# Kernel tuning notes

Measured on AMD Instinct MI355X. Metric: run time of the kernel, lower is better.

Reference implementation:

```python
import jax, jax.numpy as jnp
import numpy as np

TOPK = 10
NUM_CLASSES = 80
ALPHA = 0.5
BETA = 6.0
EPS = 1e-16


def _iou_xyxy(b1, b2):
    # b1, b2 broadcastable [..., 4] in xyxy; matches bbox_iou(xywh=False, CIoU=False)
    b1_x1, b1_y1, b1_x2, b1_y2 = b1[..., 0], b1[..., 1], b1[..., 2], b1[..., 3]
    b2_x1, b2_y1, b2_x2, b2_y2 = b2[..., 0], b2[..., 1], b2[..., 2], b2[..., 3]
    inter = jnp.clip(jnp.minimum(b1_x2, b2_x2) - jnp.maximum(b1_x1, b2_x1), 0) * \
            jnp.clip(jnp.minimum(b1_y2, b2_y2) - jnp.maximum(b1_y1, b2_y1), 0)
    w1, h1 = b1_x2 - b1_x1, b1_y2 - b1_y1 + EPS
    w2, h2 = b2_x2 - b2_x1, b2_y2 - b2_y1 + EPS
    union = w1 * h1 + w2 * h2 - inter + EPS
    return inter / union


def _assign_one(pd_s, pd_b, gt_l, gt_b, m, anc):
    # pd_s [A,C], pd_b [A,4], gt_l [N,1], gt_b [N,4], m [N,1] bool, anc [A,2]
    A = pd_s.shape[0]
    N = gt_l.shape[0]
    valid = m[:, 0]                                  # [N] padded-gt mask
    labels = gt_l[:, 0]                              # [N]
    scores = pd_s[:, labels]                         # [A,N] gather per-gt class score
    ious = _iou_xyxy(gt_b[None, :, :], pd_b[:, None, :])   # [A,N]
    align = scores ** ALPHA * ious ** BETA           # [A,N]
    # anchor-center-inside-gt test
    lt = anc[:, None, :] - gt_b[None, :, :2]         # [A,N,2]
    rb = gt_b[None, :, 2:] - anc[:, None, :]         # [A,N,2]
    in_gts = jnp.concatenate([lt, rb], axis=-1).min(axis=-1) > 0  # [A,N]
    amf = align * in_gts                             # align_metric_filter
    amf = jnp.where(valid[None, :], amf, 0.0)        # padded gts contribute nothing
    # top-k anchors per gt (over anchor dim)
    topk_idx = jax.lax.top_k(amf.T, TOPK)[1]         # [N,TOPK]
    mask_topk = jnp.zeros((N, A), dtype=bool).at[jnp.arange(N)[:, None], topk_idx].set(True).T  # [A,N]
    mask_pos = mask_topk & in_gts & valid[None, :]   # [A,N]
    fg = mask_pos.any(axis=1)                        # [A]
    # argmax over valid gts (padded columns pushed below any valid amf >= 0)
    amf_arg = jnp.where(valid[None, :], amf, -1.0)
    gt_idx = jnp.argmax(amf_arg, axis=1)             # [A]
    t_labels = jnp.where(fg, labels[gt_idx], NUM_CLASSES).astype(jnp.int32)
    t_bboxes = jnp.where(fg[:, None], gt_b[gt_idx], 0.0)
    am_max = jnp.clip(jnp.max(amf_arg, axis=1), 0.0)  # [A]
    BIG = jnp.float32(1e30)
    mn = jnp.min(jnp.where(fg, am_max, BIG))
    mx = jnp.max(jnp.where(fg, am_max, -BIG))
    norm = (am_max - mn) / (mx - mn + 1e-9)
    onehot = jax.nn.one_hot(t_labels, NUM_CLASSES, dtype=pd_s.dtype)  # label==C -> all-zero row
    t_scores = jnp.where(fg[:, None], onehot * norm[:, None], 0.0)
    return t_labels, t_bboxes, t_scores, fg


def setup_inputs() -> dict:
    key = jax.random.key(0)
    B, A, N, C = 32, 8400, 64, NUM_CLASSES
    ks = jax.random.split(key, 8)
    pd_scores = jax.random.uniform(ks[0], (B, A, C), dtype=jnp.float32)
    xy1 = jax.random.uniform(ks[1], (B, A, 2), dtype=jnp.float32) * 600.0
    wh = jax.random.uniform(ks[2], (B, A, 2), dtype=jnp.float32) * 60.0 + 4.0
    pd_bboxes = jnp.concatenate([xy1, xy1 + wh], axis=-1)
    anc_points = jax.random.uniform(ks[3], (A, 2), dtype=jnp.float32) * 640.0
    gxy1 = jax.random.uniform(ks[4], (B, N, 2), dtype=jnp.float32) * 500.0
    gwh = jax.random.uniform(ks[5], (B, N, 2), dtype=jnp.float32) * 140.0 + 20.0
    gt_bboxes = jnp.concatenate([gxy1, gxy1 + gwh], axis=-1)
    gt_labels = jax.random.randint(ks[6], (B, N, 1), 0, C, dtype=jnp.int32)
    counts = jax.random.randint(ks[7], (B,), 1, N + 1)
    mask_gt = (jnp.arange(N)[None, :] < counts[:, None])[..., None]  # [B,N,1] bool
    return {"pd_scores": pd_scores, "pd_bboxes": pd_bboxes, "anc_points": anc_points,
            "gt_labels": gt_labels, "gt_bboxes": gt_bboxes, "mask_gt": mask_gt}


def reference(pd_scores, pd_bboxes, anc_points, gt_labels, gt_bboxes, mask_gt):
    return jax.vmap(_assign_one, in_axes=(0, 0, 0, 0, 0, None))(
        pd_scores, pd_bboxes, gt_labels, gt_bboxes, mask_gt, anc_points)
```

## Files before the change

kernel.cpp:

```cpp
#include <hip/hip_runtime.h>

#define A_N 8400
#define B_N 32
#define NGT 64
#define NC  80
#define BA  (B_N * A_N)
#define NCOL (B_N * NGT)

typedef float f4 __attribute__((ext_vector_type(4)));

__global__ __launch_bounds__(256) void k_init(int* __restrict__ cnts,
                                              unsigned* __restrict__ mn_g,
                                              unsigned* __restrict__ mx_g) {
  int tid = threadIdx.x;
  for (int i = tid; i < NCOL; i += 256) cnts[i] = 0;
  if (tid < B_N) {
    mn_g[tid] = __float_as_uint(1e30f);
    mx_g[tid] = 0u;
  }
}

__global__ __launch_bounds__(256) void k_pairs(
    const float* __restrict__ pd_s, const float* __restrict__ pd_b,
    const float* __restrict__ anc, const int* __restrict__ gt_l,
    const float* __restrict__ gt_b, const int* __restrict__ mgt,
    unsigned long long* __restrict__ lists, int* __restrict__ cnts, int cap,
    unsigned long long* __restrict__ recs) {
#pragma clang fp contract(off)
  int b = blockIdx.y, tid = threadIdx.x;
  int a0 = blockIdx.x * 256, a = a0 + tid;
  bool av = a < A_N;

  __shared__ float4 gb_s[NGT];
  __shared__ int lab_s[NGT];
  __shared__ float4 pb_s[256];
  __shared__ unsigned long long key_s[256];
  __shared__ unsigned short wl[256 * 64];
  __shared__ int wl_cnt;
  __shared__ int cnt_sh;

  if (tid < NGT) {
    gb_s[tid] = ((const float4*)gt_b)[b * NGT + tid];
    lab_s[tid] = gt_l[b * NGT + tid];
    unsigned long long m = __ballot(mgt[b * NGT + tid] != 0);
    if (tid == 0) cnt_sh = __popcll(m);
  }
  float4 pb = av ? ((const float4*)pd_b)[(size_t)b * A_N + a]
                 : make_float4(0.f, 0.f, 0.f, 0.f);
  float2 ap = av ? ((const float2*)anc)[a] : make_float2(-1e30f, -1e30f);
  pb_s[tid] = pb;
  key_s[tid] = (unsigned long long)(63 << 1);
  if (tid == 0) wl_cnt = 0;
  __syncthreads();
  int cnt = cnt_sh;

  if (av) {
    for (int n = 0; n < cnt; n++) {
      float4 gb = gb_s[n];
      float mn = fminf(fminf(ap.x - gb.x, ap.y - gb.y),
                       fminf(gb.z - ap.x, gb.w - ap.y));
      float iwr = fminf(gb.z, pb.z) - fmaxf(gb.x, pb.x);
      float ihr = fminf(gb.w, pb.w) - fmaxf(gb.y, pb.y);
      if (mn > 0.0f && iwr > 0.0f && ihr > 0.0f) {
        int p = atomicAdd(&wl_cnt, 1);
        wl[p] = (unsigned short)((tid << 6) | n);
      }
    }
  }
  __syncthreads();
  int m = wl_cnt;

  for (int i = tid; i < m; i += 256) {
    int e = wl[i];
    int al = e >> 6, n = e & 63;
    int ag = a0 + al;
    float4 gb = gb_s[n];
    float4 pbl = pb_s[al];
    float iw = fmaxf(fminf(gb.z, pbl.z) - fmaxf(gb.x, pbl.x), 0.0f);
    float ih = fmaxf(fminf(gb.w, pbl.w) - fmaxf(gb.y, pbl.y), 0.0f);
    float inter = iw * ih;
    float w1 = gb.z - gb.x, h1 = (gb.w - gb.y) + 1e-16f;
    float w2 = pbl.z - pbl.x, h2 = (pbl.w - pbl.y) + 1e-16f;
    float uni = ((w1 * h1 + w2 * h2) - inter) + 1e-16f;
    float iou = inter / uni;
    float sc = pd_s[((size_t)b * A_N + ag) * NC + (size_t)lab_s[n]];
    float v = sqrtf(sc) * powf(iou, 6.0f);
    if (v > 0.0f) {
      unsigned vb = __float_as_uint(v);
      int col = b * NGT + n;
      int pos = atomicAdd(&cnts[col], 1);
      if (pos < cap) {
        lists[(size_t)col * cap + pos] =
            ((unsigned long long)vb << 32) |
            (unsigned long long)(0xFFFFFFFFu - (unsigned)ag);
      }
      atomicMax(&key_s[al], ((unsigned long long)vb << 32) |
                                (unsigned long long)((63 - n) << 1));
    }
  }
  __syncthreads();

  if (av) recs[(size_t)b * A_N + a] = key_s[tid];
}

__global__ __launch_bounds__(64) void k_topk(
    const unsigned long long* __restrict__ lists, const int* __restrict__ cnts,
    int cap, const int* __restrict__ mgt, const float* __restrict__ anc,
    const float* __restrict__ gt_b, unsigned long long* __restrict__ recs,
    unsigned* __restrict__ mn_g, unsigned* __restrict__ mx_g) {
  int b = blockIdx.x, n = blockIdx.y, tid = threadIdx.x;
  if (mgt[b * NGT + n] == 0) return;
  int col = b * NGT + n;
  int P = cnts[col];
  if (P > cap) P = cap;
  const unsigned long long* list = lists + (size_t)col * cap;
  unsigned* recw = (unsigned*)recs;

  const unsigned MN_ID = __float_as_uint(1e30f);
  unsigned loc_mn = MN_ID, loc_mx = 0u;

  if (P >= 10) {
    unsigned long long top[10];
#pragma unroll
    for (int j = 0; j < 10; j++) top[j] = 0ull;
    for (int i = tid; i < P; i += 64) {
      unsigned long long key = list[i];
#pragma unroll
      for (int j = 0; j < 10; j++) {
        if (key > top[j]) { unsigned long long t = top[j]; top[j] = key; key = t; }
      }
    }
    for (int r = 0; r < 10; r++) {
      unsigned long long g = top[0];
#pragma unroll
      for (int off = 32; off >= 1; off >>= 1) {
        unsigned long long o = __shfl_xor(g, off, 64);
        g = (o > g) ? o : g;
      }
      if (top[0] == g) {
#pragma unroll
        for (int j = 0; j < 9; j++) top[j] = top[j + 1];
        top[9] = 0ull;
      }
      if (tid == r) {
        size_t idx = (size_t)b * A_N +
                     (size_t)(0xFFFFFFFFu - (unsigned)(g & 0xFFFFFFFFull));
        atomicOr(&recw[2 * idx], 1u);
        unsigned u = recw[2 * idx + 1];
        loc_mn = (u < loc_mn) ? u : loc_mn;
        loc_mx = (u > loc_mx) ? u : loc_mx;
      }
    }
  } else {
    int my_a = -1;
    if (tid < P)
      my_a = (int)(0xFFFFFFFFu - (unsigned)(list[tid] & 0xFFFFFFFFull));
    if (tid < P) {
      size_t idx = (size_t)b * A_N + my_a;
      atomicOr(&recw[2 * idx], 1u);
      unsigned u = recw[2 * idx + 1];
      loc_mn = (u < loc_mn) ? u : loc_mn;
      loc_mx = (u > loc_mx) ? u : loc_mx;
    }
    bool is_pos = false;
    for (int i = 0; i < P; i++) {
      int ai = __shfl(my_a, i, 64);
      is_pos |= (ai == tid);
    }
    bool cand = (tid < 19) && !is_pos;
    unsigned long long fm = __ballot(cand);
    int rank = __popcll(fm & ((1ull << tid) - 1ull));
    if (cand && rank < 10 - P) {
      float4 gb = ((const float4*)gt_b)[b * NGT + n];
      float2 ap = ((const float2*)anc)[tid];
      float mn = fminf(fminf(ap.x - gb.x, ap.y - gb.y),
                       fminf(gb.z - ap.x, gb.w - ap.y));
      if (mn > 0.0f) {
        size_t idx = (size_t)b * A_N + tid;
        atomicOr(&recw[2 * idx], 1u);
        unsigned u = recw[2 * idx + 1];
        loc_mn = (u < loc_mn) ? u : loc_mn;
        loc_mx = (u > loc_mx) ? u : loc_mx;
      }
    }
  }

#pragma unroll
  for (int off = 32; off >= 1; off >>= 1) {
    unsigned o1 = __shfl_xor(loc_mn, off, 64);
    loc_mn = (o1 < loc_mn) ? o1 : loc_mn;
    unsigned o2 = __shfl_xor(loc_mx, off, 64);
    loc_mx = (o2 > loc_mx) ? o2 : loc_mx;
  }
  if (tid == 0 && loc_mn != MN_ID) {
    atomicMin(&mn_g[b], loc_mn);
    atomicMax(&mx_g[b], loc_mx);
  }
}

__global__ __launch_bounds__(256) void k_fin(
    const int* __restrict__ gt_l, const float* __restrict__ gt_b,
    const unsigned long long* __restrict__ recs,
    const unsigned* __restrict__ mn_g, const unsigned* __restrict__ mx_g,
    float* __restrict__ out) {
  int b = blockIdx.y;
  int a = blockIdx.x * 256 + threadIdx.x;
  if (a >= A_N) return;
  size_t i = (size_t)b * A_N + a;
  unsigned long long rec = recs[i];
  bool fg = (rec & 1ull) != 0;
  int bi = 63 - (int)((rec >> 1) & 63ull);
  int lab = gt_l[b * NGT + bi];

  out[i] = fg ? (float)lab : (float)NC;
  if (fg) {
    float amx = __uint_as_float((unsigned)(rec >> 32));
    float mn = __uint_as_float(mn_g[b]);
    float mx = __uint_as_float(mx_g[b]);
    float norm = (amx - mn) / ((mx - mn) + 1e-9f);
    float4 t = ((const float4*)gt_b)[b * NGT + bi];
    f4 bb = {t.x, t.y, t.z, t.w};
    ((f4*)(out + BA))[i] = bb;
    out[(size_t)85 * BA + i] = 1.0f;
    out[(size_t)5 * BA + i * NC + (size_t)lab] = norm;
  }
}

extern "C" void kernel_launch(void* const* d_in, const int* in_sizes, int n_in,
                              void* d_out, int out_size, void* d_ws,
                              size_t ws_size, hipStream_t stream) {
  const float* pd_s = (const float*)d_in[0];
  const float* pd_b = (const float*)d_in[1];
  const float* anc  = (const float*)d_in[2];
  const int*   gt_l = (const int*)d_in[3];
  const float* gt_b = (const float*)d_in[4];
  const int*   mgt  = (const int*)d_in[5];

  float* out = (float*)d_out;
  char* ws = (char*)d_ws;

  const size_t REC_BYTES = (size_t)BA * 8;
  size_t small_bytes = REC_BYTES + (size_t)NCOL * 4 + 256;
  size_t avail = (ws_size > small_bytes) ? (ws_size - small_bytes) : 0;
  int cap = (int)(avail / ((size_t)NCOL * 8));
  if (cap > 4096) cap = 4096;
  if (cap < 1) cap = 1;

  unsigned long long* lists = (unsigned long long*)ws;
  char* sb = ws + (size_t)NCOL * 8 * cap;
  unsigned long long* recs = (unsigned long long*)sb;
  int*      cnts = (int*)(sb + REC_BYTES);
  unsigned* mn_g = (unsigned*)(sb + REC_BYTES + (size_t)NCOL * 4);
  unsigned* mx_g = mn_g + B_N;

  hipMemsetAsync(out + BA, 0, (size_t)85 * BA * 4, stream);

  dim3 g2((A_N + 255) / 256, B_N);
  k_init<<<1, 256, 0, stream>>>(cnts, mn_g, mx_g);
  k_pairs<<<g2, 256, 0, stream>>>(pd_s, pd_b, anc, gt_l, gt_b, mgt, lists,
                                  cnts, cap, recs);
  k_topk<<<dim3(B_N, NGT), 64, 0, stream>>>(lists, cnts, cap, mgt, anc, gt_b,
                                            recs, mn_g, mx_g);
  k_fin<<<g2, 256, 0, stream>>>(gt_l, gt_b, recs, mn_g, mx_g, out);
}
```

Baseline: 182.9 us.

## Fuse pair, top-k and finalize stages into one cooperative kernel with grid syncs

Replaces the init, pairs, top-k and finalize kernels, plus the large output memset, with a single cooperative kernel of 512 blocks. 192 blocks zero the output with nontemporal stores while the other blocks run the pair tiles, so the zeroing overlaps the pair work. Grid-wide syncs then separate the top-k stage, where each block handles 4 columns with one wavefront each, from the finalize stage. This removes launch gaps and the separate memset pass. In exchange, it relies on all 512 blocks being co-resident and pays for two grid barriers; the min initialiser also changes from 1e30 bits to 0xFFFFFFFF.

```diff
diff --git a/kernel.cpp b/kernel.cpp
--- a/kernel.cpp
+++ b/kernel.cpp
@@ -1,4 +1,7 @@
 #include <hip/hip_runtime.h>
+#include <hip/hip_cooperative_groups.h>
+
+namespace cg = cooperative_groups;
 
 #define A_N 8400
 #define B_N 32
@@ -6,30 +9,25 @@
 #define NC  80
 #define BA  (B_N * A_N)
 #define NCOL (B_N * NGT)
+#define NBLK 512
+#define ZB   192
+#define PB   (NBLK - ZB)
+#define NTILE (33 * B_N)
+#define ZVEC ((size_t)85 * BA / 4)
 
 typedef float f4 __attribute__((ext_vector_type(4)));
 
-__global__ __launch_bounds__(256) void k_init(int* __restrict__ cnts,
-                                              unsigned* __restrict__ mn_g,
-                                              unsigned* __restrict__ mx_g) {
-  int tid = threadIdx.x;
-  for (int i = tid; i < NCOL; i += 256) cnts[i] = 0;
-  if (tid < B_N) {
-    mn_g[tid] = __float_as_uint(1e30f);
-    mx_g[tid] = 0u;
-  }
-}
-
-__global__ __launch_bounds__(256) void k_pairs(
+__global__ __launch_bounds__(256) void k_fused(
     const float* __restrict__ pd_s, const float* __restrict__ pd_b,
     const float* __restrict__ anc, const int* __restrict__ gt_l,
     const float* __restrict__ gt_b, const int* __restrict__ mgt,
     unsigned long long* __restrict__ lists, int* __restrict__ cnts, int cap,
-    unsigned long long* __restrict__ recs) {
+    unsigned long long* __restrict__ recs, unsigned* __restrict__ mn_g,
+    unsigned* __restrict__ mx_g, float* __restrict__ out) {
 #pragma clang fp contract(off)
-  int b = blockIdx.y, tid = threadIdx.x;
-  int a0 = blockIdx.x * 256, a = a0 + tid;
-  bool av = a < A_N;
+  cg::grid_group grid = cg::this_grid();
+  int tid = threadIdx.x;
+  int bk = blockIdx.x;
 
   __shared__ float4 gb_s[NGT];
   __shared__ int lab_s[NGT];
@@ -39,190 +37,201 @@
   __shared__ int wl_cnt;
   __shared__ int cnt_sh;
 
-  if (tid < NGT) {
-    gb_s[tid] = ((const float4*)gt_b)[b * NGT + tid];
-    lab_s[tid] = gt_l[b * NGT + tid];
-    unsigned long long m = __ballot(mgt[b * NGT + tid] != 0);
-    if (tid == 0) cnt_sh = __popcll(m);
-  }
-  float4 pb = av ? ((const float4*)pd_b)[(size_t)b * A_N + a]
-                 : make_float4(0.f, 0.f, 0.f, 0.f);
-  float2 ap = av ? ((const float2*)anc)[a] : make_float2(-1e30f, -1e30f);
-  pb_s[tid] = pb;
-  key_s[tid] = (unsigned long long)(63 << 1);
-  if (tid == 0) wl_cnt = 0;
-  __syncthreads();
-  int cnt = cnt_sh;
-
-  if (av) {
-    for (int n = 0; n < cnt; n++) {
-      float4 gb = gb_s[n];
-      float mn = fminf(fminf(ap.x - gb.x, ap.y - gb.y),
-                       fminf(gb.z - ap.x, gb.w - ap.y));
-      float iwr = fminf(gb.z, pb.z) - fmaxf(gb.x, pb.x);
-      float ihr = fminf(gb.w, pb.w) - fmaxf(gb.y, pb.y);
-      if (mn > 0.0f && iwr > 0.0f && ihr > 0.0f) {
-        int p = atomicAdd(&wl_cnt, 1);
-        wl[p] = (unsigned short)((tid << 6) | n);
-      }
+  if (bk < ZB) {
+    f4 z = {0.f, 0.f, 0.f, 0.f};
+    f4* dst = (f4*)(out + BA);
+    for (size_t v = (size_t)bk * 256 + tid; v < ZVEC; v += (size_t)ZB * 256)
+      __builtin_nontemporal_store(z, &dst[v]);
+  } else {
+    int pr = bk - ZB;
+    for (int t = pr; t < NTILE; t += PB) {
+      int b = t / 33, bx = t - b * 33;
+      int a0 = bx * 256, a = a0 + tid;
+      bool av = a < A_N;
+
+      if (tid < NGT) {
+        gb_s[tid] = ((const float4*)gt_b)[b * NGT + tid];
+        lab_s[tid] = gt_l[b * NGT + tid];
+        unsigned long long mm = __ballot(mgt[b * NGT + tid] != 0);
+        if (tid == 0) cnt_sh = __popcll(mm);
+      }
+      float4 pb = av ? ((const float4*)pd_b)[(size_t)b * A_N + a]
+                     : make_float4(0.f, 0.f, 0.f, 0.f);
+      float2 ap = av ? ((const float2*)anc)[a] : make_float2(-1e30f, -1e30f);
+      pb_s[tid] = pb;
+      key_s[tid] = (unsigned long long)(63 << 1);
+      if (tid == 0) wl_cnt = 0;
+      __syncthreads();
+      int cnt = cnt_sh;
+
+      if (av) {
+        for (int n = 0; n < cnt; n++) {
+          float4 gb = gb_s[n];
+          float mn = fminf(fminf(ap.x - gb.x, ap.y - gb.y),
+                           fminf(gb.z - ap.x, gb.w - ap.y));
+          float iwr = fminf(gb.z, pb.z) - fmaxf(gb.x, pb.x);
+          float ihr = fminf(gb.w, pb.w) - fmaxf(gb.y, pb.y);
+          if (mn > 0.0f && iwr > 0.0f && ihr > 0.0f) {
+            int p = atomicAdd(&wl_cnt, 1);
+            wl[p] = (unsigned short)((tid << 6) | n);
+          }
+        }
+      }
+      __syncthreads();
+      int m = wl_cnt;
+
+      for (int i = tid; i < m; i += 256) {
+        int e = wl[i];
+        int al = e >> 6, n = e & 63;
+        int ag = a0 + al;
+        float4 gb = gb_s[n];
+        float4 pbl = pb_s[al];
+        float iw = fmaxf(fminf(gb.z, pbl.z) - fmaxf(gb.x, pbl.x), 0.0f);
+        float ih = fmaxf(fminf(gb.w, pbl.w) - fmaxf(gb.y, pbl.y), 0.0f);
+        float inter = iw * ih;
+        float w1 = gb.z - gb.x, h1 = (gb.w - gb.y) + 1e-16f;
+        float w2 = pbl.z - pbl.x, h2 = (pbl.w - pbl.y) + 1e-16f;
+        float uni = ((w1 * h1 + w2 * h2) - inter) + 1e-16f;
+        float iou = inter / uni;
+        float sc = pd_s[((size_t)b * A_N + ag) * NC + (size_t)lab_s[n]];
+        float v = sqrtf(sc) * powf(iou, 6.0f);
+        if (v > 0.0f) {
+          unsigned vb = __float_as_uint(v);
+          int col = b * NGT + n;
+          int pos = atomicAdd(&cnts[col], 1);
+          if (pos < cap) {
+            lists[(size_t)col * cap + pos] =
+                ((unsigned long long)vb << 32) |
+                (unsigned long long)(0xFFFFFFFFu - (unsigned)ag);
+          }
+          atomicMax(&key_s[al], ((unsigned long long)vb << 32) |
+                                    (unsigned long long)((63 - n) << 1));
+        }
+      }
+      __syncthreads();
+      if (av) recs[(size_t)b * A_N + a] = key_s[tid];
     }
   }
-  __syncthreads();
-  int m = wl_cnt;
-
-  for (int i = tid; i < m; i += 256) {
-    int e = wl[i];
-    int al = e >> 6, n = e & 63;
-    int ag = a0 + al;
-    float4 gb = gb_s[n];
-    float4 pbl = pb_s[al];
-    float iw = fmaxf(fminf(gb.z, pbl.z) - fmaxf(gb.x, pbl.x), 0.0f);
-    float ih = fmaxf(fminf(gb.w, pbl.w) - fmaxf(gb.y, pbl.y), 0.0f);
-    float inter = iw * ih;
-    float w1 = gb.z - gb.x, h1 = (gb.w - gb.y) + 1e-16f;
-    float w2 = pbl.z - pbl.x, h2 = (pbl.w - pbl.y) + 1e-16f;
-    float uni = ((w1 * h1 + w2 * h2) - inter) + 1e-16f;
-    float iou = inter / uni;
-    float sc = pd_s[((size_t)b * A_N + ag) * NC + (size_t)lab_s[n]];
-    float v = sqrtf(sc) * powf(iou, 6.0f);
-    if (v > 0.0f) {
-      unsigned vb = __float_as_uint(v);
-      int col = b * NGT + n;
-      int pos = atomicAdd(&cnts[col], 1);
-      if (pos < cap) {
-        lists[(size_t)col * cap + pos] =
-            ((unsigned long long)vb << 32) |
-            (unsigned long long)(0xFFFFFFFFu - (unsigned)ag);
-      }
-      atomicMax(&key_s[al], ((unsigned long long)vb << 32) |
-                                (unsigned long long)((63 - n) << 1));
+
+  __threadfence();
+  grid.sync();
+
+  {
+    int lane = tid & 63;
+    int col = bk * 4 + (tid >> 6);
+    unsigned* recw = (unsigned*)recs;
+    unsigned loc_mn = 0xFFFFFFFFu, loc_mx = 0u;
+    if (mgt[col] != 0) {
+      int b = col >> 6;
+      int P = cnts[col];
+      if (P > cap) P = cap;
+      const unsigned long long* list = lists + (size_t)col * cap;
+
+      if (P >= 10) {
+        unsigned long long top[10];
+#pragma unroll
+        for (int j = 0; j < 10; j++) top[j] = 0ull;
+        for (int i = lane; i < P; i += 64) {
+          unsigned long long key = list[i];
+#pragma unroll
+          for (int j = 0; j < 10; j++) {
+            if (key > top[j]) { unsigned long long tt = top[j]; top[j] = key; key = tt; }
+          }
+        }
+        for (int r = 0; r < 10; r++) {
+          unsigned long long g = top[0];
+#pragma unroll
+          for (int off = 32; off >= 1; off >>= 1) {
+            unsigned long long o = __shfl_xor(g, off, 64);
+            g = (o > g) ? o : g;
+          }
+          if (top[0] == g) {
+#pragma unroll
+            for (int j = 0; j < 9; j++) top[j] = top[j + 1];
+            top[9] = 0ull;
+          }
+          if (lane == r) {
+            size_t idx = (size_t)b * A_N +
+                         (size_t)(0xFFFFFFFFu - (unsigned)(g & 0xFFFFFFFFull));
+            atomicOr(&recw[2 * idx], 1u);
+            unsigned u = recw[2 * idx + 1];
+            loc_mn = (u < loc_mn) ? u : loc_mn;
+            loc_mx = (u > loc_mx) ? u : loc_mx;
+          }
+        }
+      } else {
+        int my_a = -1;
+        if (lane < P)
+          my_a = (int)(0xFFFFFFFFu - (unsigned)(list[lane] & 0xFFFFFFFFull));
+        if (lane < P) {
+          size_t idx = (size_t)b * A_N + my_a;
+          atomicOr(&recw[2 * idx], 1u);
+          unsigned u = recw[2 * idx + 1];
+          loc_mn = (u < loc_mn) ? u : loc_mn;
+          loc_mx = (u > loc_mx) ? u : loc_mx;
+        }
+        bool is_pos = false;
+        for (int i = 0; i < P; i++) {
+          int ai = __shfl(my_a, i, 64);
+          is_pos |= (ai == lane);
+        }
+        bool cand = (lane < 19) && !is_pos;
+        unsigned long long fm = __ballot(cand);
+        int rank = __popcll(fm & ((1ull << lane) - 1ull));
+        if (cand && rank < 10 - P) {
+          int n = col & 63;
+          float4 gb = ((const float4*)gt_b)[b * NGT + n];
+          float2 ap = ((const float2*)anc)[lane];
+          float mn = fminf(fminf(ap.x - gb.x, ap.y - gb.y),
+                           fminf(gb.z - ap.x, gb.w - ap.y));
+          if (mn > 0.0f) {
+            size_t idx = (size_t)b * A_N + lane;
+            atomicOr(&recw[2 * idx], 1u);
+            unsigned u = recw[2 * idx + 1];
+            loc_mn = (u < loc_mn) ? u : loc_mn;
+            loc_mx = (u > loc_mx) ? u : loc_mx;
+          }
+        }
+      }
+#pragma unroll
+      for (int off = 32; off >= 1; off >>= 1) {
+        unsigned o1 = __shfl_xor(loc_mn, off, 64);
+        loc_mn = (o1 < loc_mn) ? o1 : loc_mn;
+        unsigned o2 = __shfl_xor(loc_mx, off, 64);
+        loc_mx = (o2 > loc_mx) ? o2 : loc_mx;
+      }
+      if (lane == 0 && loc_mn != 0xFFFFFFFFu) {
+        atomicMin(&mn_g[b], loc_mn);
+        atomicMax(&mx_g[b], loc_mx);
+      }
     }
   }
-  __syncthreads();
-
-  if (av) recs[(size_t)b * A_N + a] = key_s[tid];
-}
-
-__global__ __launch_bounds__(64) void k_topk(
-    const unsigned long long* __restrict__ lists, const int* __restrict__ cnts,
-    int cap, const int* __restrict__ mgt, const float* __restrict__ anc,
-    const float* __restrict__ gt_b, unsigned long long* __restrict__ recs,
-    unsigned* __restrict__ mn_g, unsigned* __restrict__ mx_g) {
-  int b = blockIdx.x, n = blockIdx.y, tid = threadIdx.x;
-  if (mgt[b * NGT + n] == 0) return;
-  int col = b * NGT + n;
-  int P = cnts[col];
-  if (P > cap) P = cap;
-  const unsigned long long* list = lists + (size_t)col * cap;
-  unsigned* recw = (unsigned*)recs;
-
-  const unsigned MN_ID = __float_as_uint(1e30f);
-  unsigned loc_mn = MN_ID, loc_mx = 0u;
-
-  if (P >= 10) {
-    unsigned long long top[10];
-#pragma unroll
-    for (int j = 0; j < 10; j++) top[j] = 0ull;
-    for (int i = tid; i < P; i += 64) {
-      unsigned long long key = list[i];
-#pragma unroll
-      for (int j = 0; j < 10; j++) {
-        if (key > top[j]) { unsigned long long t = top[j]; top[j] = key; key = t; }
+
+  __threadfence();
+  grid.sync();
+
+  for (int t = bk; t < NTILE; t += NBLK) {
+    int b = t / 33, bx = t - b * 33;
+    int a = bx * 256 + tid;
+    if (a < A_N) {
+      size_t i = (size_t)b * A_N + a;
+      unsigned long long rec = recs[i];
+      bool fg = (rec & 1ull) != 0;
+      int bi = 63 - (int)((rec >> 1) & 63ull);
+      int lab = gt_l[b * NGT + bi];
+      out[i] = fg ? (float)lab : (float)NC;
+      if (fg) {
+        float amx = __uint_as_float((unsigned)(rec >> 32));
+        float mn = __uint_as_float(mn_g[b]);
+        float mx = __uint_as_float(mx_g[b]);
+        float norm = (amx - mn) / ((mx - mn) + 1e-9f);
+        float4 tt = ((const float4*)gt_b)[b * NGT + bi];
+        f4 bb = {tt.x, tt.y, tt.z, tt.w};
+        ((f4*)(out + BA))[i] = bb;
+        out[(size_t)85 * BA + i] = 1.0f;
+        out[(size_t)5 * BA + i * NC + (size_t)lab] = norm;
       }
     }
-    for (int r = 0; r < 10; r++) {
-      unsigned long long g = top[0];
-#pragma unroll
-      for (int off = 32; off >= 1; off >>= 1) {
-        unsigned long long o = __shfl_xor(g, off, 64);
-        g = (o > g) ? o : g;
-      }
-      if (top[0] == g) {
-#pragma unroll
-        for (int j = 0; j < 9; j++) top[j] = top[j + 1];
-        top[9] = 0ull;
-      }
-      if (tid == r) {
-        size_t idx = (size_t)b * A_N +
-                     (size_t)(0xFFFFFFFFu - (unsigned)(g & 0xFFFFFFFFull));
-        atomicOr(&recw[2 * idx], 1u);
-        unsigned u = recw[2 * idx + 1];
-        loc_mn = (u < loc_mn) ? u : loc_mn;
-        loc_mx = (u > loc_mx) ? u : loc_mx;
-      }
-    }
-  } else {
-    int my_a = -1;
-    if (tid < P)
-      my_a = (int)(0xFFFFFFFFu - (unsigned)(list[tid] & 0xFFFFFFFFull));
-    if (tid < P) {
-      size_t idx = (size_t)b * A_N + my_a;
-      atomicOr(&recw[2 * idx], 1u);
-      unsigned u = recw[2 * idx + 1];
-      loc_mn = (u < loc_mn) ? u : loc_mn;
-      loc_mx = (u > loc_mx) ? u : loc_mx;
-    }
-    bool is_pos = false;
-    for (int i = 0; i < P; i++) {
-      int ai = __shfl(my_a, i, 64);
-      is_pos |= (ai == tid);
-    }
-    bool cand = (tid < 19) && !is_pos;
-    unsigned long long fm = __ballot(cand);
-    int rank = __popcll(fm & ((1ull << tid) - 1ull));
-    if (cand && rank < 10 - P) {
-      float4 gb = ((const float4*)gt_b)[b * NGT + n];
-      float2 ap = ((const float2*)anc)[tid];
-      float mn = fminf(fminf(ap.x - gb.x, ap.y - gb.y),
-                       fminf(gb.z - ap.x, gb.w - ap.y));
-      if (mn > 0.0f) {
-        size_t idx = (size_t)b * A_N + tid;
-        atomicOr(&recw[2 * idx], 1u);
-        unsigned u = recw[2 * idx + 1];
-        loc_mn = (u < loc_mn) ? u : loc_mn;
-        loc_mx = (u > loc_mx) ? u : loc_mx;
-      }
-    }
-  }
-
-#pragma unroll
-  for (int off = 32; off >= 1; off >>= 1) {
-    unsigned o1 = __shfl_xor(loc_mn, off, 64);
-    loc_mn = (o1 < loc_mn) ? o1 : loc_mn;
-    unsigned o2 = __shfl_xor(loc_mx, off, 64);
-    loc_mx = (o2 > loc_mx) ? o2 : loc_mx;
-  }
-  if (tid == 0 && loc_mn != MN_ID) {
-    atomicMin(&mn_g[b], loc_mn);
-    atomicMax(&mx_g[b], loc_mx);
-  }
-}
-
-__global__ __launch_bounds__(256) void k_fin(
-    const int* __restrict__ gt_l, const float* __restrict__ gt_b,
-    const unsigned long long* __restrict__ recs,
-    const unsigned* __restrict__ mn_g, const unsigned* __restrict__ mx_g,
-    float* __restrict__ out) {
-  int b = blockIdx.y;
-  int a = blockIdx.x * 256 + threadIdx.x;
-  if (a >= A_N) return;
-  size_t i = (size_t)b * A_N + a;
-  unsigned long long rec = recs[i];
-  bool fg = (rec & 1ull) != 0;
-  int bi = 63 - (int)((rec >> 1) & 63ull);
-  int lab = gt_l[b * NGT + bi];
-
-  out[i] = fg ? (float)lab : (float)NC;
-  if (fg) {
-    float amx = __uint_as_float((unsigned)(rec >> 32));
-    float mn = __uint_as_float(mn_g[b]);
-    float mx = __uint_as_float(mx_g[b]);
-    float norm = (amx - mn) / ((mx - mn) + 1e-9f);
-    float4 t = ((const float4*)gt_b)[b * NGT + bi];
-    f4 bb = {t.x, t.y, t.z, t.w};
-    ((f4*)(out + BA))[i] = bb;
-    out[(size_t)85 * BA + i] = 1.0f;
-    out[(size_t)5 * BA + i * NC + (size_t)lab] = norm;
   }
 }
 
@@ -250,16 +259,16 @@
   char* sb = ws + (size_t)NCOL * 8 * cap;
   unsigned long long* recs = (unsigned long long*)sb;
   int*      cnts = (int*)(sb + REC_BYTES);
-  unsigned* mn_g = (unsigned*)(sb + REC_BYTES + (size_t)NCOL * 4);
-  unsigned* mx_g = mn_g + B_N;
-
-  hipMemsetAsync(out + BA, 0, (size_t)85 * BA * 4, stream);
-
-  dim3 g2((A_N + 255) / 256, B_N);
-  k_init<<<1, 256, 0, stream>>>(cnts, mn_g, mx_g);
-  k_pairs<<<g2, 256, 0, stream>>>(pd_s, pd_b, anc, gt_l, gt_b, mgt, lists,
-                                  cnts, cap, recs);
-  k_topk<<<dim3(B_N, NGT), 64, 0, stream>>>(lists, cnts, cap, mgt, anc, gt_b,
-                                            recs, mn_g, mx_g);
-  k_fin<<<g2, 256, 0, stream>>>(gt_l, gt_b, recs, mn_g, mx_g, out);
+  unsigned* mx_g = (unsigned*)(sb + REC_BYTES + (size_t)NCOL * 4);
+  unsigned* mn_g = mx_g + B_N;
+
+  hipMemsetAsync(cnts, 0, (size_t)NCOL * 4 + (size_t)B_N * 4, stream);
+  hipMemsetAsync(mn_g, 0xFF, (size_t)B_N * 4, stream);
+
+  void* kargs[] = {(void*)&pd_s, (void*)&pd_b, (void*)&anc,  (void*)&gt_l,
+                   (void*)&gt_b, (void*)&mgt,  (void*)&lists, (void*)&cnts,
+                   (void*)&cap,  (void*)&recs, (void*)&mn_g, (void*)&mx_g,
+                   (void*)&out};
+  hipLaunchCooperativeKernel((const void*)k_fused, dim3(NBLK), dim3(256),
+                             kargs, 0, stream);
 }
```

After: 412.5 us. 2.26x slower.
